# Performance work log

Hardware: AMD Instinct MI355X
Metric: run time of the kernel (lower is better)

The kernel has to match this reference:

```python
import jax, jax.numpy as jnp
import numpy as np

D_MODEL = 300   # hardcoded d_model1 in Matposer.__init__
VOCAB = 32000
B, L = 512, 512
OUT = 4


def sinusoidal_pe(length, d):
    # Standard 'Attention is All You Need' positional encoding used by the repo's PositionalEncoding.
    pos = jnp.arange(length, dtype=jnp.float32)[:, None]
    div = jnp.exp(jnp.arange(0, d, 2, dtype=jnp.float32) * (-np.log(10000.0) / d))
    pe = jnp.zeros((length, d), dtype=jnp.float32)
    pe = pe.at[:, 0::2].set(jnp.sin(pos * div))
    pe = pe.at[:, 1::2].set(jnp.cos(pos * div))
    return pe


def setup_inputs() -> dict:
    key = jax.random.key(0)
    k1, k2, k3, k4, k5, k6 = jax.random.split(key, 6)
    return {
        "x1": jax.random.randint(k1, (B, L), 0, VOCAB, dtype=jnp.int32),
        "x2": jax.random.randint(k2, (B, L), 0, VOCAB, dtype=jnp.int32),
        "emb1": jax.random.normal(k3, (VOCAB, D_MODEL), dtype=jnp.float32) * 0.02,
        "emb2": jax.random.normal(k4, (VOCAB, D_MODEL), dtype=jnp.float32) * 0.02,
        "w1": jax.random.normal(k5, (D_MODEL, D_MODEL), dtype=jnp.float32) / np.sqrt(D_MODEL),
        "b1": jnp.zeros((D_MODEL,), dtype=jnp.float32),
        "w2": jax.random.normal(k6, (OUT, D_MODEL), dtype=jnp.float32) / np.sqrt(D_MODEL),
        "b2": jnp.zeros((OUT,), dtype=jnp.float32),
    }


def reference(x1, x2, emb1, emb2, w1, b1, w2, b2):
    scale = jnp.sqrt(jnp.float32(D_MODEL))   # Embeddings multiplies by sqrt(d_model)
    pe = sinusoidal_pe(x1.shape[1], D_MODEL)  # [L, D]
    # Embed + positional encoding (dropout=0 / eval mode). [B, L, D]
    e1 = emb1[x1] * scale + pe
    e2 = emb2[x2] * scale + pe
    # encoded_sents = e2.permute(0,2,1) @ e1 -> [B, D, D]
    fmap = jnp.einsum('bld,ble->bde', e2, e1)
    # torch Tensor.diagonal() defaults to dim1=0, dim2=1 -> shape [D, min(B, D)]
    diag = jnp.diagonal(fmap, axis1=0, axis2=1)  # [D, D] since B >= D
    # class_fc: Linear(300,300) -> ReLU -> Linear(300,output_size); torch Linear: x @ W.T + b
    h = jax.nn.relu(diag @ w1.T + b1)
    logits = h @ w2.T + b2
    # nn.Softmax() on a 2D input -> softmax over dim=1
    return jax.nn.softmax(logits, axis=-1)
```

## Files before the change

### kernel.cpp

```cpp
#include <hip/hip_runtime.h>
#include <math.h>

#define D_MODEL 300
#define LSEQ    512
#define NBATCH  300
#define SPLIT   16
#define LCH     (LSEQ / SPLIT)
#define NG      4
#define LPG     (LCH / NG)
#define NR      75
#define KCH     (D_MODEL / 4)
#define JPB     2
#define TI      6
#define SPLITB  16
#define LCHB    (LSEQ / SPLITB)
#define SCALE   17.32050807568877f

__global__ void pe_kernel(float* __restrict__ pe) {
    int idx = blockIdx.x * blockDim.x + threadIdx.x;
    if (idx >= LSEQ * D_MODEL) return;
    int l = idx / D_MODEL;
    int e = idx - l * D_MODEL;
    int k = e >> 1;
    float dv = expf((float)(2 * k) * (-9.210340371976184f / 300.0f));
    float arg = (float)l * dv;
    pe[idx] = (e & 1) ? cosf(arg) : sinf(arg);
}

__global__ void s_kernel(const int* __restrict__ x2, const float* __restrict__ emb2,
                         const float* __restrict__ pe, float* __restrict__ S) {
    int idx = blockIdx.x * blockDim.x + threadIdx.x;
    if (idx >= NBATCH * LSEQ) return;
    int i = idx >> 9;
    int l = idx & (LSEQ - 1);
    int v = x2[idx];
    S[idx] = emb2[(size_t)v * D_MODEL + i] * SCALE + pe[l * D_MODEL + i];
}

__global__ void diagA_kernel(const int* __restrict__ x1, const float* __restrict__ S,
                             const float* __restrict__ emb1, float* __restrict__ Dm) {
    __shared__ int    x1ch[LCH];
    __shared__ float  sch[LCH];
    __shared__ float4 part[NG][NR];
    const int i   = blockIdx.x;
    const int sp  = blockIdx.y;
    const int tid = threadIdx.x;
    const int l0  = sp * LCH;

    if (tid < LCH) {
        x1ch[tid] = x1[i * LSEQ + l0 + tid];
        sch[tid]  = S[i * LSEQ + l0 + tid] * SCALE;
    }
    __syncthreads();

    const int g = tid / NR;
    const int r = tid - g * NR;

    if (tid < NG * NR) {
        const int lb = g * LPG;
        const float4 v0 = ((const float4*)(emb1 + (size_t)x1ch[lb + 0] * D_MODEL))[r];
        const float4 v1 = ((const float4*)(emb1 + (size_t)x1ch[lb + 1] * D_MODEL))[r];
        const float4 v2 = ((const float4*)(emb1 + (size_t)x1ch[lb + 2] * D_MODEL))[r];
        const float4 v3 = ((const float4*)(emb1 + (size_t)x1ch[lb + 3] * D_MODEL))[r];
        const float4 v4 = ((const float4*)(emb1 + (size_t)x1ch[lb + 4] * D_MODEL))[r];
        const float4 v5 = ((const float4*)(emb1 + (size_t)x1ch[lb + 5] * D_MODEL))[r];
        const float4 v6 = ((const float4*)(emb1 + (size_t)x1ch[lb + 6] * D_MODEL))[r];
        const float4 v7 = ((const float4*)(emb1 + (size_t)x1ch[lb + 7] * D_MODEL))[r];
        const float s0 = sch[lb + 0], s1 = sch[lb + 1], s2 = sch[lb + 2], s3 = sch[lb + 3];
        const float s4 = sch[lb + 4], s5 = sch[lb + 5], s6 = sch[lb + 6], s7 = sch[lb + 7];
        float ax, ay, az, aw;
        ax = s0 * v0.x;            ay = s0 * v0.y;            az = s0 * v0.z;            aw = s0 * v0.w;
        ax = fmaf(s1, v1.x, ax);   ay = fmaf(s1, v1.y, ay);   az = fmaf(s1, v1.z, az);   aw = fmaf(s1, v1.w, aw);
        ax = fmaf(s2, v2.x, ax);   ay = fmaf(s2, v2.y, ay);   az = fmaf(s2, v2.z, az);   aw = fmaf(s2, v2.w, aw);
        ax = fmaf(s3, v3.x, ax);   ay = fmaf(s3, v3.y, ay);   az = fmaf(s3, v3.z, az);   aw = fmaf(s3, v3.w, aw);
        ax = fmaf(s4, v4.x, ax);   ay = fmaf(s4, v4.y, ay);   az = fmaf(s4, v4.z, az);   aw = fmaf(s4, v4.w, aw);
        ax = fmaf(s5, v5.x, ax);   ay = fmaf(s5, v5.y, ay);   az = fmaf(s5, v5.z, az);   aw = fmaf(s5, v5.w, aw);
        ax = fmaf(s6, v6.x, ax);   ay = fmaf(s6, v6.y, ay);   az = fmaf(s6, v6.z, az);   aw = fmaf(s6, v6.w, aw);
        ax = fmaf(s7, v7.x, ax);   ay = fmaf(s7, v7.y, ay);   az = fmaf(s7, v7.z, az);   aw = fmaf(s7, v7.w, aw);
        part[g][r] = make_float4(ax, ay, az, aw);
    }
    __syncthreads();

    if (g == 0 && tid < NR) {
        float4 p0 = part[0][r], p1 = part[1][r], p2 = part[2][r], p3 = part[3][r];
        float* dst = Dm + i * D_MODEL + 4 * r;
        atomicAdd(dst + 0, p0.x + p1.x + p2.x + p3.x);
        atomicAdd(dst + 1, p0.y + p1.y + p2.y + p3.y);
        atomicAdd(dst + 2, p0.z + p1.z + p2.z + p3.z);
        atomicAdd(dst + 3, p0.w + p1.w + p2.w + p3.w);
    }
}

__global__ void termB_kernel(const float* __restrict__ S, const float* __restrict__ pe,
                             float* __restrict__ Dm) {
    __shared__ float sS[TI][LCHB];
    const int i0  = blockIdx.x * TI;
    const int l0  = blockIdx.y * LCHB;
    const int tid = threadIdx.x;

    if (tid < TI * LCHB) {
        int ti = tid >> 5;
        int l  = tid & (LCHB - 1);
        sS[ti][l] = S[(i0 + ti) * LSEQ + l0 + l];
    }
    __syncthreads();

    if (tid < D_MODEL) {
        float acc0 = 0.f, acc1 = 0.f, acc2 = 0.f, acc3 = 0.f, acc4 = 0.f, acc5 = 0.f;
        #pragma unroll
        for (int l = 0; l < LCHB; l += 4) {
            float p0 = pe[(l0 + l + 0) * D_MODEL + tid];
            float p1 = pe[(l0 + l + 1) * D_MODEL + tid];
            float p2 = pe[(l0 + l + 2) * D_MODEL + tid];
            float p3 = pe[(l0 + l + 3) * D_MODEL + tid];
            acc0 = fmaf(sS[0][l + 0], p0, acc0); acc0 = fmaf(sS[0][l + 1], p1, acc0);
            acc0 = fmaf(sS[0][l + 2], p2, acc0); acc0 = fmaf(sS[0][l + 3], p3, acc0);
            acc1 = fmaf(sS[1][l + 0], p0, acc1); acc1 = fmaf(sS[1][l + 1], p1, acc1);
            acc1 = fmaf(sS[1][l + 2], p2, acc1); acc1 = fmaf(sS[1][l + 3], p3, acc1);
            acc2 = fmaf(sS[2][l + 0], p0, acc2); acc2 = fmaf(sS[2][l + 1], p1, acc2);
            acc2 = fmaf(sS[2][l + 2], p2, acc2); acc2 = fmaf(sS[2][l + 3], p3, acc2);
            acc3 = fmaf(sS[3][l + 0], p0, acc3); acc3 = fmaf(sS[3][l + 1], p1, acc3);
            acc3 = fmaf(sS[3][l + 2], p2, acc3); acc3 = fmaf(sS[3][l + 3], p3, acc3);
            acc4 = fmaf(sS[4][l + 0], p0, acc4); acc4 = fmaf(sS[4][l + 1], p1, acc4);
            acc4 = fmaf(sS[4][l + 2], p2, acc4); acc4 = fmaf(sS[4][l + 3], p3, acc4);
            acc5 = fmaf(sS[5][l + 0], p0, acc5); acc5 = fmaf(sS[5][l + 1], p1, acc5);
            acc5 = fmaf(sS[5][l + 2], p2, acc5); acc5 = fmaf(sS[5][l + 3], p3, acc5);
        }
        atomicAdd(&Dm[(i0 + 0) * D_MODEL + tid], acc0);
        atomicAdd(&Dm[(i0 + 1) * D_MODEL + tid], acc1);
        atomicAdd(&Dm[(i0 + 2) * D_MODEL + tid], acc2);
        atomicAdd(&Dm[(i0 + 3) * D_MODEL + tid], acc3);
        atomicAdd(&Dm[(i0 + 4) * D_MODEL + tid], acc4);
        atomicAdd(&Dm[(i0 + 5) * D_MODEL + tid], acc5);
    }
}

__global__ void fc1_kernel(const float* __restrict__ w1, const float* __restrict__ Dm,
                           float* __restrict__ Hpre) {
    const int j0  = blockIdx.x * JPB;
    const int sp  = blockIdx.y;
    const int tid = threadIdx.x;
    const int k0  = sp * KCH;
    if (tid >= D_MODEL) return;
    const float* w1r0 = w1 + (j0 + 0) * D_MODEL + k0;
    const float* w1r1 = w1 + (j0 + 1) * D_MODEL + k0;
    float acc0 = 0.0f, acc1 = 0.0f;
    #pragma unroll 5
    for (int k = 0; k < KCH; ++k) {
        float d = Dm[(k0 + k) * D_MODEL + tid];
        acc0 = fmaf(w1r0[k], d, acc0);
        acc1 = fmaf(w1r1[k], d, acc1);
    }
    atomicAdd(&Hpre[(j0 + 0) * D_MODEL + tid], acc0);
    atomicAdd(&Hpre[(j0 + 1) * D_MODEL + tid], acc1);
}

__global__ void fc2_softmax_kernel(const float* __restrict__ Hpre, const float* __restrict__ b1,
                                   const float* __restrict__ w2, const float* __restrict__ b2,
                                   float* __restrict__ out) {
    __shared__ float sm[4][4][64];
    const int tid   = threadIdx.x;
    const int e_loc = tid & 63;
    const int jc    = tid >> 6;
    const int e     = blockIdx.x * 64 + e_loc;

    float a0 = 0.f, a1 = 0.f, a2 = 0.f, a3 = 0.f;
    if (e < D_MODEL) {
        const int j0 = jc * 75;
        #pragma unroll 5
        for (int j = j0; j < j0 + 75; ++j) {
            float h = fmaxf(Hpre[j * D_MODEL + e] + b1[j], 0.0f);
            a0 = fmaf(h, w2[0 * D_MODEL + j], a0);
            a1 = fmaf(h, w2[1 * D_MODEL + j], a1);
            a2 = fmaf(h, w2[2 * D_MODEL + j], a2);
            a3 = fmaf(h, w2[3 * D_MODEL + j], a3);
        }
    }
    sm[jc][0][e_loc] = a0; sm[jc][1][e_loc] = a1;
    sm[jc][2][e_loc] = a2; sm[jc][3][e_loc] = a3;
    __syncthreads();

    if (jc == 0 && e < D_MODEL) {
        float l0 = b2[0] + sm[0][0][e_loc] + sm[1][0][e_loc] + sm[2][0][e_loc] + sm[3][0][e_loc];
        float l1 = b2[1] + sm[0][1][e_loc] + sm[1][1][e_loc] + sm[2][1][e_loc] + sm[3][1][e_loc];
        float l2 = b2[2] + sm[0][2][e_loc] + sm[1][2][e_loc] + sm[2][2][e_loc] + sm[3][2][e_loc];
        float l3 = b2[3] + sm[0][3][e_loc] + sm[1][3][e_loc] + sm[2][3][e_loc] + sm[3][3][e_loc];
        float m  = fmaxf(fmaxf(l0, l1), fmaxf(l2, l3));
        float x0 = expf(l0 - m), x1 = expf(l1 - m), x2 = expf(l2 - m), x3 = expf(l3 - m);
        float inv = 1.0f / (x0 + x1 + x2 + x3);
        out[e * 4 + 0] = x0 * inv;
        out[e * 4 + 1] = x1 * inv;
        out[e * 4 + 2] = x2 * inv;
        out[e * 4 + 3] = x3 * inv;
    }
}

extern "C" void kernel_launch(void* const* d_in, const int* in_sizes, int n_in,
                              void* d_out, int out_size, void* d_ws, size_t ws_size,
                              hipStream_t stream) {
    const int*   x1   = (const int*)d_in[0];
    const int*   x2   = (const int*)d_in[1];
    const float* emb1 = (const float*)d_in[2];
    const float* emb2 = (const float*)d_in[3];
    const float* w1   = (const float*)d_in[4];
    const float* b1   = (const float*)d_in[5];
    const float* w2   = (const float*)d_in[6];
    const float* b2   = (const float*)d_in[7];
    float* out = (float*)d_out;

    char* ws = (char*)d_ws;
    float* pe   = (float*)ws;
    float* Dm   = (float*)(ws + 614400);
    float* Hpre = (float*)(ws + 974400);
    float* S    = (float*)(ws + 1334400);

    (void)hipMemsetAsync(Dm, 0, 2 * 360000, stream);

    pe_kernel<<<(LSEQ * D_MODEL + 255) / 256, 256, 0, stream>>>(pe);
    s_kernel<<<(NBATCH * LSEQ + 255) / 256, 256, 0, stream>>>(x2, emb2, pe, S);
    diagA_kernel<<<dim3(NBATCH, SPLIT), 320, 0, stream>>>(x1, S, emb1, Dm);
    termB_kernel<<<dim3(NBATCH / TI, SPLITB), 320, 0, stream>>>(S, pe, Dm);
    fc1_kernel<<<dim3(D_MODEL / JPB, 4), 320, 0, stream>>>(w1, Dm, Hpre);
    fc2_softmax_kernel<<<(D_MODEL + 63) / 64, 256, 0, stream>>>(Hpre, b1, w2, b2, out);
}
```

Before: 169.2 us.

## Fuse S computation into consumers, drop memset, and remove fc1 split-K atomics

Removes the separate S kernel by recomputing the emb2 gather plus positional encoding inside both diagA and termB. Zeroing Dm moves into pe_kernel, replacing the memset. fc1 now computes the full K reduction per block with fused bias and ReLU, which removes the atomics and the need to zero Hpre. termB uses half as many L splits, so each block handles longer chunks. The change trades a few kernel launches and atomic traffic for duplicated gathers and less parallelism in fc1 and termB.

```diff
diff --git a/kernel.cpp b/kernel.cpp
--- a/kernel.cpp
+++ b/kernel.cpp
@@ -9,15 +9,14 @@
 #define NG      4
 #define LPG     (LCH / NG)
 #define NR      75
-#define KCH     (D_MODEL / 4)
-#define JPB     2
 #define TI      6
-#define SPLITB  16
+#define SPLITB  8
 #define LCHB    (LSEQ / SPLITB)
 #define SCALE   17.32050807568877f
 
-__global__ void pe_kernel(float* __restrict__ pe) {
+__global__ void pe_kernel(float* __restrict__ pe, float* __restrict__ Dm) {
     int idx = blockIdx.x * blockDim.x + threadIdx.x;
+    if (idx < D_MODEL * D_MODEL) Dm[idx] = 0.0f;
     if (idx >= LSEQ * D_MODEL) return;
     int l = idx / D_MODEL;
     int e = idx - l * D_MODEL;
@@ -27,18 +26,9 @@
     pe[idx] = (e & 1) ? cosf(arg) : sinf(arg);
 }
 
-__global__ void s_kernel(const int* __restrict__ x2, const float* __restrict__ emb2,
-                         const float* __restrict__ pe, float* __restrict__ S) {
-    int idx = blockIdx.x * blockDim.x + threadIdx.x;
-    if (idx >= NBATCH * LSEQ) return;
-    int i = idx >> 9;
-    int l = idx & (LSEQ - 1);
-    int v = x2[idx];
-    S[idx] = emb2[(size_t)v * D_MODEL + i] * SCALE + pe[l * D_MODEL + i];
-}
-
-__global__ void diagA_kernel(const int* __restrict__ x1, const float* __restrict__ S,
-                             const float* __restrict__ emb1, float* __restrict__ Dm) {
+__global__ void diagA_kernel(const int* __restrict__ x1, const int* __restrict__ x2,
+                             const float* __restrict__ emb1, const float* __restrict__ emb2,
+                             const float* __restrict__ pe, float* __restrict__ Dm) {
     __shared__ int    x1ch[LCH];
     __shared__ float  sch[LCH];
     __shared__ float4 part[NG][NR];
@@ -48,8 +38,10 @@
     const int l0  = sp * LCH;
 
     if (tid < LCH) {
-        x1ch[tid] = x1[i * LSEQ + l0 + tid];
-        sch[tid]  = S[i * LSEQ + l0 + tid] * SCALE;
+        const int l = l0 + tid;
+        x1ch[tid] = x1[i * LSEQ + l];
+        const int v2 = x2[i * LSEQ + l];
+        sch[tid] = (emb2[(size_t)v2 * D_MODEL + i] * SCALE + pe[l * D_MODEL + i]) * SCALE;
     }
     __syncthreads();
 
@@ -91,23 +83,26 @@
     }
 }
 
-__global__ void termB_kernel(const float* __restrict__ S, const float* __restrict__ pe,
-                             float* __restrict__ Dm) {
+__global__ void termB_kernel(const int* __restrict__ x2, const float* __restrict__ emb2,
+                             const float* __restrict__ pe, float* __restrict__ Dm) {
     __shared__ float sS[TI][LCHB];
     const int i0  = blockIdx.x * TI;
     const int l0  = blockIdx.y * LCHB;
     const int tid = threadIdx.x;
 
-    if (tid < TI * LCHB) {
-        int ti = tid >> 5;
-        int l  = tid & (LCHB - 1);
-        sS[ti][l] = S[(i0 + ti) * LSEQ + l0 + l];
+    for (int t = tid; t < TI * LCHB; t += 320) {
+        const int ti = t >> 6;
+        const int l  = t & (LCHB - 1);
+        const int gi = i0 + ti;
+        const int gl = l0 + l;
+        const int v2 = x2[gi * LSEQ + gl];
+        sS[ti][l] = emb2[(size_t)v2 * D_MODEL + gi] * SCALE + pe[gl * D_MODEL + gi];
     }
     __syncthreads();
 
     if (tid < D_MODEL) {
         float acc0 = 0.f, acc1 = 0.f, acc2 = 0.f, acc3 = 0.f, acc4 = 0.f, acc5 = 0.f;
-        #pragma unroll
+        #pragma unroll 8
         for (int l = 0; l < LCHB; l += 4) {
             float p0 = pe[(l0 + l + 0) * D_MODEL + tid];
             float p1 = pe[(l0 + l + 1) * D_MODEL + tid];
@@ -136,28 +131,21 @@
 }
 
 __global__ void fc1_kernel(const float* __restrict__ w1, const float* __restrict__ Dm,
-                           float* __restrict__ Hpre) {
-    const int j0  = blockIdx.x * JPB;
-    const int sp  = blockIdx.y;
+                           const float* __restrict__ b1, float* __restrict__ Hpre) {
+    const int j   = blockIdx.x;
     const int tid = threadIdx.x;
-    const int k0  = sp * KCH;
     if (tid >= D_MODEL) return;
-    const float* w1r0 = w1 + (j0 + 0) * D_MODEL + k0;
-    const float* w1r1 = w1 + (j0 + 1) * D_MODEL + k0;
-    float acc0 = 0.0f, acc1 = 0.0f;
-    #pragma unroll 5
-    for (int k = 0; k < KCH; ++k) {
-        float d = Dm[(k0 + k) * D_MODEL + tid];
-        acc0 = fmaf(w1r0[k], d, acc0);
-        acc1 = fmaf(w1r1[k], d, acc1);
-    }
-    atomicAdd(&Hpre[(j0 + 0) * D_MODEL + tid], acc0);
-    atomicAdd(&Hpre[(j0 + 1) * D_MODEL + tid], acc1);
-}
-
-__global__ void fc2_softmax_kernel(const float* __restrict__ Hpre, const float* __restrict__ b1,
-                                   const float* __restrict__ w2, const float* __restrict__ b2,
-                                   float* __restrict__ out) {
+    const float* w1r = w1 + j * D_MODEL;
+    float acc = 0.0f;
+    #pragma unroll 4
+    for (int k = 0; k < D_MODEL; ++k) {
+        acc = fmaf(w1r[k], Dm[k * D_MODEL + tid], acc);
+    }
+    Hpre[j * D_MODEL + tid] = fmaxf(acc + b1[j], 0.0f);
+}
+
+__global__ void fc2_softmax_kernel(const float* __restrict__ Hpre, const float* __restrict__ w2,
+                                   const float* __restrict__ b2, float* __restrict__ out) {
     __shared__ float sm[4][4][64];
     const int tid   = threadIdx.x;
     const int e_loc = tid & 63;
@@ -169,7 +157,7 @@
         const int j0 = jc * 75;
         #pragma unroll 5
         for (int j = j0; j < j0 + 75; ++j) {
-            float h = fmaxf(Hpre[j * D_MODEL + e] + b1[j], 0.0f);
+            float h = Hpre[j * D_MODEL + e];
             a0 = fmaf(h, w2[0 * D_MODEL + j], a0);
             a1 = fmaf(h, w2[1 * D_MODEL + j], a1);
             a2 = fmaf(h, w2[2 * D_MODEL + j], a2);
@@ -212,14 +200,10 @@
     float* pe   = (float*)ws;
     float* Dm   = (float*)(ws + 614400);
     float* Hpre = (float*)(ws + 974400);
-    float* S    = (float*)(ws + 1334400);
-
-    (void)hipMemsetAsync(Dm, 0, 2 * 360000, stream);
-
-    pe_kernel<<<(LSEQ * D_MODEL + 255) / 256, 256, 0, stream>>>(pe);
-    s_kernel<<<(NBATCH * LSEQ + 255) / 256, 256, 0, stream>>>(x2, emb2, pe, S);
-    diagA_kernel<<<dim3(NBATCH, SPLIT), 320, 0, stream>>>(x1, S, emb1, Dm);
-    termB_kernel<<<dim3(NBATCH / TI, SPLITB), 320, 0, stream>>>(S, pe, Dm);
-    fc1_kernel<<<dim3(D_MODEL / JPB, 4), 320, 0, stream>>>(w1, Dm, Hpre);
-    fc2_softmax_kernel<<<(D_MODEL + 63) / 64, 256, 0, stream>>>(Hpre, b1, w2, b2, out);
-}
+
+    pe_kernel<<<(LSEQ * D_MODEL + 255) / 256, 256, 0, stream>>>(pe, Dm);
+    diagA_kernel<<<dim3(NBATCH, SPLIT), 320, 0, stream>>>(x1, x2, emb1, emb2, pe, Dm);
+    termB_kernel<<<dim3(NBATCH / TI, SPLITB), 320, 0, stream>>>(x2, emb2, pe, Dm);
+    fc1_kernel<<<NBATCH, 320, 0, stream>>>(w1, Dm, b1, Hpre);
+    fc2_softmax_kernel<<<(D_MODEL + 63) / 64, 256, 0, stream>>>(Hpre, w2, b2, out);
+}
```

New measurement: 179.2 us. +5.9%, slower.
